# Kernel tuning notes

Measured on AMD Instinct MI355X. Metric: run time of the kernel, lower is better.

Reference implementation:

```python
import jax, jax.numpy as jnp
import numpy as np

MARGIN = 0.2
SCALE = 30.0

def setup_inputs() -> dict:
    key = jax.random.key(0)
    k1, k2 = jax.random.split(key)
    B, D, C = 8192, 512, 100
    embeddings = jax.random.normal(k1, (B, D), dtype=jnp.float32)
    labels = jax.random.randint(k2, (B,), 0, C, dtype=jnp.int64)
    return {"embeddings": embeddings, "labels": labels}

def reference(embeddings, labels):
    # Cosine similarity via one GEMM: normalize rows once, then n @ n.T.
    # (torch F.cosine_similarity uses eps=1e-8 on norms)
    norms = jnp.maximum(jnp.linalg.norm(embeddings, axis=1, keepdims=True), 1e-8)
    n = embeddings / norms                      # [B, D]
    sim = n @ n.T                               # [B, B]
    pos_mask = labels[:, None] == labels[None, :]  # includes diagonal, as in original
    e = jnp.exp(SCALE * (sim - MARGIN))         # [B, B]
    pos_sum = jnp.sum(jnp.where(pos_mask, e, 0.0))
    neg_sum = jnp.sum(jnp.where(pos_mask, 0.0, e))
    loss = jnp.log1p(neg_sum / pos_sum)
    return loss
```

## Files before the change

kernel.cpp:

```cpp
#include <hip/hip_runtime.h>
#include <hip/hip_bf16.h>
#include <math.h>


#define BDIM 8192
#define DDIM 512
#define MARGIN 0.2f
#define SCALE 30.0f

#define BT 256
#define BK 32
#define NKT (DDIM / BK)
#define NT (BDIM / BT)
#define NBLK (NT * (NT + 1) / 2)

typedef __hip_bfloat16 bf16;
using f32x4  = __attribute__((ext_vector_type(4))) float;
using bf16x8 = __attribute__((ext_vector_type(8))) short;
using us8    = __attribute__((ext_vector_type(8))) unsigned short;

#define GLOAD_LDS16(gp, lp)                                                    \
    __builtin_amdgcn_global_load_lds(                                          \
        (const __attribute__((address_space(1))) unsigned int*)(gp),           \
        (__attribute__((address_space(3))) unsigned int*)(lp), 16, 0, 0)

__device__ __forceinline__ unsigned short f2bf(float x) {
    union { bf16 h; unsigned short u; } c;
    c.h = __float2bfloat16(x);
    return c.u;
}

__global__ __launch_bounds__(256)
void norm_rows_kernel(const float* __restrict__ emb, bf16* __restrict__ nout,
                      double* __restrict__ accum, unsigned* __restrict__ ctr) {
    if (blockIdx.x == 0 && threadIdx.x == 0) {
        accum[0] = 0.0; accum[1] = 0.0; *ctr = 0u;
    }
    const int row  = blockIdx.x * 4 + (threadIdx.x >> 6);
    const int lane = threadIdx.x & 63;
    const float4* src = (const float4*)(emb + (size_t)row * DDIM) + lane * 2;
    const float4 a = src[0];
    const float4 b = src[1];
    float ss = a.x * a.x + a.y * a.y + a.z * a.z + a.w * a.w
             + b.x * b.x + b.y * b.y + b.z * b.z + b.w * b.w;
    #pragma unroll
    for (int off = 1; off < 64; off <<= 1) ss += __shfl_xor(ss, off, 64);
    const float inv = 1.0f / fmaxf(sqrtf(ss), 1e-8f);
    float v[8] = { a.x, a.y, a.z, a.w, b.x, b.y, b.z, b.w };
    us8 o;
    #pragma unroll
    for (int i = 0; i < 8; ++i) o[i] = f2bf(v[i] * inv);
    *((us8*)(nout + (size_t)row * DDIM) + lane) = o;
}

__global__ __launch_bounds__(512)
void gemm_loss_kernel(const bf16* __restrict__ nmat,
                      const int* __restrict__ labels,
                      double* __restrict__ accum, unsigned* __restrict__ ctr,
                      float* __restrict__ out) {
    const int hw = blockIdx.x;
    const int l = (hw & 7) * (NBLK / 8) + (hw >> 3);
    auto tri = [](int b) { return ((65 - b) * b) >> 1; };
    int bi = (int)((65.0 - sqrt(4225.0 - 8.0 * (double)l)) * 0.5);
    bi = bi < 0 ? 0 : (bi > 31 ? 31 : bi);
    while (bi > 0 && tri(bi) > l) --bi;
    while (tri(bi + 1) <= l) ++bi;
    const int bj = bi + (l - tri(bi));

    __shared__ alignas(16) short As[4][BT * BK];
    __shared__ alignas(16) short Bs[4][BT * BK];
    __shared__ int lr[BT], lc[BT];
    __shared__ double red[16];

    const int tix = threadIdx.x, wid = tix >> 6, lane = tix & 63;
    if (tix < 256) lr[tix] = labels[bi * BT + tix];
    else           lc[tix - 256] = labels[bj * BT + (tix - 256)];

    const int wm = wid >> 2;
    const int wn = wid & 3;

    const int srow = wid * 16 + (lane >> 2);
    const int scol = ((lane & 3) ^ ((lane >> 3) & 3)) * 8;
    const bf16* gA = nmat + (size_t)(bi * BT + srow) * DDIM + scol;
    const bf16* gB = nmat + (size_t)(bj * BT + srow) * DDIM + scol;
    const int ldst = wid * 16 * BK;

    #define STG_A(buf, kt, h)                                                  \
        GLOAD_LDS16(gA + (size_t)((h) * 128) * DDIM + (kt) * BK,               \
                    &As[buf][(h) * 128 * BK + ldst])
    #define STG_B(buf, kt, h)                                                  \
        GLOAD_LDS16(gB + (size_t)((h) * 128) * DDIM + (kt) * BK,               \
                    &Bs[buf][(h) * 128 * BK + ldst])

    const int aoff  = (lane & 15) * BK + (((lane >> 4) ^ ((lane >> 1) & 3)) * 8);
    const int abase = wm * 128 * BK;
    const int bbase = wn * 64 * BK;

    f32x4 acc[8][4] = {};

    #pragma unroll
    for (int tt = 0; tt < 3; ++tt) {
        STG_A(tt, tt, 0); STG_A(tt, tt, 1);
        STG_B(tt, tt, 0); STG_B(tt, tt, 1);
    }

    #pragma unroll
    for (int t = 0; t < NKT; ++t) {
        const int cur = t & 3, pre = (t + 3) & 3;
        if (t <= NKT - 3)      { asm volatile("s_waitcnt vmcnt(8)" ::: "memory"); }
        else if (t == NKT - 2) { asm volatile("s_waitcnt vmcnt(4)" ::: "memory"); }
        else                   { asm volatile("s_waitcnt vmcnt(0)" ::: "memory"); }
        __builtin_amdgcn_s_barrier();
        asm volatile("" ::: "memory");
        if (t < NKT - 3) {
            STG_A(pre, t + 3, 0); STG_A(pre, t + 3, 1);
            STG_B(pre, t + 3, 0); STG_B(pre, t + 3, 1);
        }
        bf16x8 a[8], b[4];
        #pragma unroll
        for (int m = 0; m < 8; ++m)
            a[m] = *(const bf16x8*)&As[cur][abase + m * (16 * BK) + aoff];
        #pragma unroll
        for (int n = 0; n < 4; ++n)
            b[n] = *(const bf16x8*)&Bs[cur][bbase + n * (16 * BK) + aoff];
        __builtin_amdgcn_s_setprio(1);
        #pragma unroll
        for (int m = 0; m < 8; ++m)
            #pragma unroll
            for (int n = 0; n < 4; ++n)
                acc[m][n] = __builtin_amdgcn_mfma_f32_16x16x32_bf16(
                    a[m], b[n], acc[m][n], 0, 0, 0);
        __builtin_amdgcn_s_setprio(0);
    }
    #undef STG_A
    #undef STG_B

    float posf = 0.0f, negf = 0.0f;
    const int rbase = wm * 128 + (lane >> 4) * 4;
    const int cbase = wn * 64 + (lane & 15);
    #pragma unroll
    for (int m = 0; m < 8; ++m) {
        #pragma unroll
        for (int n = 0; n < 4; ++n) {
            const int ljv = lc[cbase + n * 16];
            #pragma unroll
            for (int r = 0; r < 4; ++r) {
                const float e = __expf(fmaf(acc[m][n][r], SCALE, -SCALE * MARGIN));
                if (lr[rbase + m * 16 + r] == ljv) posf += e; else negf += e;
            }
        }
    }

    double dp = (double)posf, dn = (double)negf;
    #pragma unroll
    for (int o = 32; o > 0; o >>= 1) {
        dp += __shfl_down(dp, o, 64);
        dn += __shfl_down(dn, o, 64);
    }
    if (lane == 0) { red[wid * 2] = dp; red[wid * 2 + 1] = dn; }
    __syncthreads();
    if (tix == 0) {
        const double w = (bi == bj) ? 1.0 : 2.0;
        double p = 0.0, q = 0.0;
        #pragma unroll
        for (int i = 0; i < 8; ++i) { p += red[2 * i]; q += red[2 * i + 1]; }
        atomicAdd(&accum[0], p * w);
        atomicAdd(&accum[1], q * w);
        __threadfence();
        unsigned prev = atomicAdd(ctr, 1u);
        if (prev == NBLK - 1) {
            __threadfence();
            double pp = atomicAdd(&accum[0], 0.0);
            double qq = atomicAdd(&accum[1], 0.0);
            out[0] = (float)log1p(qq / pp);
        }
    }
}

extern "C" void kernel_launch(void* const* d_in, const int* in_sizes, int n_in,
                              void* d_out, int out_size, void* d_ws, size_t ws_size,
                              hipStream_t stream) {
    const float* emb  = (const float*)d_in[0];
    const int* labels = (const int*)d_in[1];
    float* out        = (float*)d_out;

    double* accum = (double*)d_ws;
    unsigned* ctr = (unsigned*)((char*)d_ws + 16);
    bf16* nmat    = (bf16*)((char*)d_ws + 256);

    norm_rows_kernel<<<BDIM / 4, 256, 0, stream>>>(emb, nmat, accum, ctr);
    gemm_loss_kernel<<<NBLK, 512, 0, stream>>>(nmat, labels, accum, ctr, out);
}
```

Measured before the change: 136.7 us.

## Restructure GEMM main loop into double-buffered BK=64 with register prefetch

Replaces the 4-stage BK=32 LDS ring with 2 buffers of two 32-wide k-halves each, giving an effective BK of 64. The LDS fragment reads for the next half are issued into a second register set while MFMAs run on the current set, with barriers placed around each MFMA burst to interleave the waves. The aim is to hide LDS read latency behind MFMA work and halve the number of outer iterations. In exchange it adds more barriers per iteration, a shallower global prefetch, and extra registers for two fragment sets, which may lower occupancy.

```diff
diff --git a/kernel.cpp b/kernel.cpp
--- a/kernel.cpp
+++ b/kernel.cpp
@@ -9,7 +9,7 @@
 #define SCALE 30.0f
 
 #define BT 256
-#define BK 32
+#define BK 64
 #define NKT (DDIM / BK)
 #define NT (BDIM / BT)
 #define NBLK (NT * (NT + 1) / 2)
@@ -67,8 +67,8 @@
     while (tri(bi + 1) <= l) ++bi;
     const int bj = bi + (l - tri(bi));
 
-    __shared__ alignas(16) short As[4][BT * BK];
-    __shared__ alignas(16) short Bs[4][BT * BK];
+    __shared__ alignas(16) short As[2][2][256 * 32];
+    __shared__ alignas(16) short Bs[2][2][256 * 32];
     __shared__ int lr[BT], lc[BT];
     __shared__ double red[16];
 
@@ -83,57 +83,84 @@
     const int scol = ((lane & 3) ^ ((lane >> 3) & 3)) * 8;
     const bf16* gA = nmat + (size_t)(bi * BT + srow) * DDIM + scol;
     const bf16* gB = nmat + (size_t)(bj * BT + srow) * DDIM + scol;
-    const int ldst = wid * 16 * BK;
-
-    #define STG_A(buf, kt, h)                                                  \
-        GLOAD_LDS16(gA + (size_t)((h) * 128) * DDIM + (kt) * BK,               \
-                    &As[buf][(h) * 128 * BK + ldst])
-    #define STG_B(buf, kt, h)                                                  \
-        GLOAD_LDS16(gB + (size_t)((h) * 128) * DDIM + (kt) * BK,               \
-                    &Bs[buf][(h) * 128 * BK + ldst])
-
-    const int aoff  = (lane & 15) * BK + (((lane >> 4) ^ ((lane >> 1) & 3)) * 8);
-    const int abase = wm * 128 * BK;
-    const int bbase = wn * 64 * BK;
+    const int ldst = (wid * 16) * 32;
+
+    #define STG_S(buf, kt, kk)                                                 \
+        do {                                                                   \
+            GLOAD_LDS16(gA + (kt) * 64 + (kk) * 32, &As[buf][kk][ldst]);       \
+            GLOAD_LDS16(gA + (size_t)128 * DDIM + (kt) * 64 + (kk) * 32,       \
+                        &As[buf][kk][128 * 32 + ldst]);                        \
+            GLOAD_LDS16(gB + (kt) * 64 + (kk) * 32, &Bs[buf][kk][ldst]);       \
+            GLOAD_LDS16(gB + (size_t)128 * DDIM + (kt) * 64 + (kk) * 32,       \
+                        &Bs[buf][kk][128 * 32 + ldst]);                        \
+        } while (0)
+
+    const int swzc = (((lane >> 4) ^ ((lane >> 1) & 3)) * 8);
+    const int arw  = (lane & 15) * 32 + swzc;
+
+    #define READ_U(buf, kk, ua, ub)                                            \
+        do {                                                                   \
+            _Pragma("unroll")                                                  \
+            for (int m = 0; m < 8; ++m)                                        \
+                ua[m] = *(const bf16x8*)&As[buf][kk][(wm * 128 + m * 16) * 32 + arw]; \
+            _Pragma("unroll")                                                  \
+            for (int n = 0; n < 4; ++n)                                        \
+                ub[n] = *(const bf16x8*)&Bs[buf][kk][(wn * 64 + n * 16) * 32 + arw];  \
+        } while (0)
+
+    #define MFMA32(ua, ub)                                                     \
+        do {                                                                   \
+            __builtin_amdgcn_s_setprio(1);                                     \
+            _Pragma("unroll")                                                  \
+            for (int m = 0; m < 8; ++m)                                        \
+                _Pragma("unroll")                                              \
+                for (int n = 0; n < 4; ++n)                                    \
+                    acc[m][n] = __builtin_amdgcn_mfma_f32_16x16x32_bf16(       \
+                        ua[m], ub[n], acc[m][n], 0, 0, 0);                     \
+            __builtin_amdgcn_s_setprio(0);                                     \
+        } while (0)
+
+    #define BAR()                                                              \
+        do {                                                                   \
+            asm volatile("" ::: "memory");                                     \
+            __builtin_amdgcn_s_barrier();                                      \
+            asm volatile("" ::: "memory");                                     \
+        } while (0)
 
     f32x4 acc[8][4] = {};
-
-    #pragma unroll
-    for (int tt = 0; tt < 3; ++tt) {
-        STG_A(tt, tt, 0); STG_A(tt, tt, 1);
-        STG_B(tt, tt, 0); STG_B(tt, tt, 1);
-    }
+    bf16x8 u0a[8], u0b[4], u1a[8], u1b[4];
+
+    STG_S(0, 0, 0);
+    STG_S(0, 0, 1);
+    STG_S(1, 1, 0);
+    asm volatile("s_waitcnt vmcnt(8)" ::: "memory");
+    __syncthreads();
+    READ_U(0, 0, u0a, u0b);
 
     #pragma unroll
     for (int t = 0; t < NKT; ++t) {
-        const int cur = t & 3, pre = (t + 3) & 3;
-        if (t <= NKT - 3)      { asm volatile("s_waitcnt vmcnt(8)" ::: "memory"); }
-        else if (t == NKT - 2) { asm volatile("s_waitcnt vmcnt(4)" ::: "memory"); }
-        else                   { asm volatile("s_waitcnt vmcnt(0)" ::: "memory"); }
-        __builtin_amdgcn_s_barrier();
-        asm volatile("" ::: "memory");
-        if (t < NKT - 3) {
-            STG_A(pre, t + 3, 0); STG_A(pre, t + 3, 1);
-            STG_B(pre, t + 3, 0); STG_B(pre, t + 3, 1);
+        const int cur = t & 1, nxt = cur ^ 1;
+        if (t + 1 < NKT) STG_S(nxt, t + 1, 1);
+        if (t < NKT - 1) { asm volatile("s_waitcnt vmcnt(8)" ::: "memory"); }
+        else             { asm volatile("s_waitcnt vmcnt(0)" ::: "memory"); }
+        READ_U(cur, 1, u1a, u1b);
+        BAR();
+        MFMA32(u0a, u0b);
+        BAR();
+        if (t + 2 < NKT) STG_S(cur, t + 2, 0);
+        if (t + 1 < NKT) {
+            if (t + 2 < NKT) { asm volatile("s_waitcnt vmcnt(8)" ::: "memory"); }
+            else             { asm volatile("s_waitcnt vmcnt(4)" ::: "memory"); }
+            READ_U(nxt, 0, u0a, u0b);
         }
-        bf16x8 a[8], b[4];
-        #pragma unroll
-        for (int m = 0; m < 8; ++m)
-            a[m] = *(const bf16x8*)&As[cur][abase + m * (16 * BK) + aoff];
-        #pragma unroll
-        for (int n = 0; n < 4; ++n)
-            b[n] = *(const bf16x8*)&Bs[cur][bbase + n * (16 * BK) + aoff];
-        __builtin_amdgcn_s_setprio(1);
-        #pragma unroll
-        for (int m = 0; m < 8; ++m)
-            #pragma unroll
-            for (int n = 0; n < 4; ++n)
-                acc[m][n] = __builtin_amdgcn_mfma_f32_16x16x32_bf16(
-                    a[m], b[n], acc[m][n], 0, 0, 0);
-        __builtin_amdgcn_s_setprio(0);
-    }
-    #undef STG_A
-    #undef STG_B
+        BAR();
+        MFMA32(u1a, u1b);
+        BAR();
+    }
+    #undef STG_S
+    #undef READ_U
+    #undef MFMA32
+    #undef BAR
 
     float posf = 0.0f, negf = 0.0f;
     const int rbase = wm * 128 + (lane >> 4) * 4;
```

After: 144.7 us. +5.9%, slower.
